# Kernel optimization log

Hardware: AMD Instinct MI355X
Metric: run time of the kernel (lower is better)

## Reference

```python
import jax, jax.numpy as jnp
import numpy as np
import math

D_MODEL = 1024
N_HEADS = 16
HEAD_DIM = 64
BATCH = 2
SEQ = 2048


def setup_inputs() -> dict:
    key = jax.random.key(0)
    ks = jax.random.split(key, 5)
    x = jax.random.normal(ks[0], (BATCH, SEQ, D_MODEL), dtype=jnp.float32)
    s = 0.02
    wq = jax.random.normal(ks[1], (D_MODEL, D_MODEL), dtype=jnp.float32) * s
    wk = jax.random.normal(ks[2], (D_MODEL, D_MODEL), dtype=jnp.float32) * s
    wv = jax.random.normal(ks[3], (D_MODEL, D_MODEL), dtype=jnp.float32) * s
    wo = jax.random.normal(ks[4], (D_MODEL, D_MODEL), dtype=jnp.float32) * s
    gammas = jnp.linspace(0.9, 0.99, N_HEADS, dtype=jnp.float32)
    return {"x": x, "wq": wq, "wk": wk, "wv": wv, "wo": wo, "gammas": gammas}


def _decay_mask(length: int, gammas: jnp.ndarray, dtype) -> jnp.ndarray:
    # [H, L, L]: gamma^(t-s) for t >= s, else 0 (causal exponential decay)
    pos = jnp.arange(length)
    diff = pos[:, None] - pos[None, :]
    causal = diff >= 0
    d = jnp.maximum(diff, 0).astype(dtype)
    g = gammas.astype(dtype)[:, None, None]
    return jnp.where(causal[None], jnp.power(g, d[None]), jnp.zeros((), dtype))


def reference(x, wq, wk, wv, wo, gammas):
    B, L, D = x.shape
    H, hd = N_HEADS, HEAD_DIM
    # torch nn.Linear: y = x @ W.T
    q = (x @ wq.T).reshape(B, L, H, hd)
    k = (x @ wk.T).reshape(B, L, H, hd)
    v = (x @ wv.T).reshape(B, L, H, hd)
    scale = 1.0 / math.sqrt(hd)
    scores = jnp.einsum('bthd,bshd->bhts', q * scale, k)  # [B,H,L,L]
    decay = _decay_mask(L, gammas, x.dtype)               # [H,L,L]
    weights = scores * decay[None]
    retained = jnp.einsum('bhts,bshd->bthd', weights, v)  # [B,L,H,hd]
    return retained.reshape(B, L, H * hd) @ wo.T
```

## Files before the change

kernel.cpp:

```cpp
#include <hip/hip_runtime.h>


typedef __attribute__((ext_vector_type(8))) short bf16x8;
typedef __attribute__((ext_vector_type(4))) float f32x4;
typedef __attribute__((ext_vector_type(16))) float f32x16;
typedef __attribute__((ext_vector_type(4))) unsigned short u16x4;
typedef __attribute__((ext_vector_type(8))) unsigned short u16x8;
typedef __attribute__((ext_vector_type(4))) unsigned int u32x4;

__device__ inline unsigned short f2bf(float f) {
    unsigned int u;
    __builtin_memcpy(&u, &f, 4);
    u += 0x7fffu + ((u >> 16) & 1u);
    return (unsigned short)(u >> 16);
}

__device__ inline f32x4 mfma16(bf16x8 a, bf16x8 b, f32x4 c) {
    return __builtin_amdgcn_mfma_f32_16x16x32_bf16(a, b, c, 0, 0, 0);
}
__device__ inline f32x16 mfma32(bf16x8 a, bf16x8 b, f32x16 c) {
    return __builtin_amdgcn_mfma_f32_32x32x16_bf16(a, b, c, 0, 0, 0);
}

__device__ inline void gl16(const unsigned short* g, unsigned short* l) {
    __builtin_amdgcn_global_load_lds(
        (const __attribute__((address_space(1))) unsigned int*)g,
        (__attribute__((address_space(3))) unsigned int*)l,
        16, 0, 0);
}

__device__ inline unsigned cvtpk(float lo, float hi) {
    unsigned r;
    asm("v_cvt_pk_bf16_f32 %0, %1, %2" : "=v"(r) : "v"(lo), "v"(hi));
    return r;
}

__global__ __launch_bounds__(256) void convert_bf16(
    const float* __restrict__ x,
    const float* __restrict__ wq, const float* __restrict__ wk,
    const float* __restrict__ wv, const float* __restrict__ wo,
    unsigned short* __restrict__ xb,
    unsigned short* __restrict__ wqb, unsigned short* __restrict__ wkb,
    unsigned short* __restrict__ wvb, unsigned short* __restrict__ wob)
{
    int cid = blockIdx.x * 256 + threadIdx.x;
    #pragma unroll
    for (int it = 0; it < 4; ++it, cid += 262144) {
        const float* src;
        unsigned short* dst;
        size_t off;
        if (cid < 524288) {
            src = x; dst = xb; off = (size_t)cid * 8;
        } else {
            const int t = cid - 524288;
            const int seg = t >> 17;
            off = (size_t)(t & 131071) * 8;
            src = seg == 0 ? wq : seg == 1 ? wk : seg == 2 ? wv : wo;
            dst = seg == 0 ? wqb : seg == 1 ? wkb : seg == 2 ? wvb : wob;
        }
        f32x4 a = *(const f32x4*)(src + off);
        f32x4 b = *(const f32x4*)(src + off + 4);
        u32x4 v = { cvtpk(a[0], a[1]), cvtpk(a[2], a[3]),
                    cvtpk(b[0], b[1]), cvtpk(b[2], b[3]) };
        *(u32x4*)(dst + off) = v;
    }
}

__global__ __launch_bounds__(256) void qkv_bf16(
    const unsigned short* __restrict__ xb,
    const unsigned short* __restrict__ wqb, const unsigned short* __restrict__ wkb,
    const unsigned short* __restrict__ wvb,
    unsigned short* __restrict__ qfr, unsigned short* __restrict__ kfr,
    unsigned short* __restrict__ vfr)
{
    __shared__ unsigned short sR[128 * 64];
    __shared__ unsigned short sL[128 * 64];

    const int z = blockIdx.z;
    const unsigned short* W = (z == 0) ? wqb : (z == 1) ? wkb : wvb;
    const unsigned short* Rs = (z < 2) ? xb : W;
    const unsigned short* Ls = (z < 2) ? W : xb;
    const int rblk = (z < 2) ? blockIdx.x : blockIdx.y;
    const int lblk = (z < 2) ? blockIdx.y : blockIdx.x;

    const int tid = threadIdx.x;
    const int l = tid & 63, w = tid >> 6;
    const int lrow = l & 15, koff4 = (l >> 4) * 4;
    const int swz = lrow & 7;
    const int wrow = (w >> 1) * 64, wcol = (w & 1) * 64;

    f32x4 acc[4][4] = {};

    const int srow = w * 32 + (l >> 3);
    const int scol = ((l & 7) ^ ((l >> 3) & 7)) * 8;
    const unsigned short* gR = Rs + (size_t)(rblk * 128 + srow) * 1024 + scol;
    const unsigned short* gL = Ls + (size_t)(lblk * 128 + srow) * 1024 + scol;
    unsigned short* lRb = sR + (w * 32) * 64;
    unsigned short* lLb = sL + (w * 32) * 64;

    for (int kk = 0; kk < 1024; kk += 64) {
        #pragma unroll
        for (int p = 0; p < 4; ++p) {
            gl16(gR + (size_t)p * 8 * 1024 + kk, lRb + p * 512);
            gl16(gL + (size_t)p * 8 * 1024 + kk, lLb + p * 512);
        }
        __syncthreads();
        #pragma unroll
        for (int kt = 0; kt < 2; ++kt) {
            bf16x8 aL[4], bR[4];
            #pragma unroll
            for (int f = 0; f < 4; ++f) {
                const int co = ((kt * 4 + (l >> 4)) ^ swz) * 8;
                aL[f] = *(const bf16x8*)&sL[(wcol + f * 16 + lrow) * 64 + co];
                bR[f] = *(const bf16x8*)&sR[(wrow + f * 16 + lrow) * 64 + co];
            }
            #pragma unroll
            for (int af = 0; af < 4; ++af)
                #pragma unroll
                for (int bf = 0; bf < 4; ++bf)
                    acc[af][bf] = mfma16(aL[af], bR[bf], acc[af][bf]);
        }
        __syncthreads();
    }

    #pragma unroll
    for (int af = 0; af < 4; ++af) {
        #pragma unroll
        for (int bf = 0; bf < 4; ++bf) {
            const int m = rblk * 128 + wrow + bf * 16 + lrow;
            const int n0 = lblk * 128 + wcol + af * 16 + koff4;
            f32x4 v = acc[af][bf];
            unsigned p0 = cvtpk(v[0], v[1]), p1 = cvtpk(v[2], v[3]);
            u16x4 val = { (unsigned short)(p0 & 0xffff), (unsigned short)(p0 >> 16),
                          (unsigned short)(p1 & 0xffff), (unsigned short)(p1 >> 16) };
            if (z < 2) {
                const int bq = m >> 11, s = m & 2047;
                const int h2 = n0 >> 6, dd = n0 & 63;
                const size_t addr = (size_t)((bq * 16 + h2) * 64 + (s >> 5)) * 2048
                                  + (size_t)(dd >> 4) * 512 + (size_t)((dd >> 3) & 1) * 256
                                  + (size_t)(s & 31) * 8 + (dd & 7);
                unsigned short* dst = z ? kfr : qfr;
                *(u16x4*)(dst + addr) = val;
            } else {
                const int h2 = m >> 6, dd = m & 63;
                const int bq = n0 >> 11, t = n0 & 2047;
                const size_t addr = (size_t)((bq * 16 + h2) * 64 + (t >> 5)) * 2048
                                  + (size_t)((dd >> 5) * 2 + ((t >> 4) & 1)) * 512
                                  + (size_t)((t >> 3) & 1) * 256
                                  + (size_t)(dd & 31) * 8 + (t & 7);
                *(u16x4*)(vfr + addr) = val;
            }
        }
    }
}

__global__ __launch_bounds__(256) void retention_paired(
    const unsigned short* __restrict__ qfr, const unsigned short* __restrict__ kfr,
    const unsigned short* __restrict__ vfr, const float* __restrict__ gammas,
    unsigned short* __restrict__ ret)
{
    __shared__ float red[3][32][64];

    const int bid = blockIdx.x;
    const int xcd = bid & 7;
    const int j = bid >> 3;
    const int m = j >> 5;
    const int p = j & 31;
    const int b = m >> 1;
    const int pi = b ? (7 - xcd) : xcd;
    const int h = (m & 1) ? (15 - pi) : pi;
    const float lg = log2f(gammas[h]);
    const int cut_i = (int)(45.0f / (-lg));
    const float gi32 = exp2f(-32.0f * lg);

    const int tid = threadIdx.x;
    const int l = tid & 63, w = tid >> 6;
    const int l31 = l & 31, hi = l >> 5;

    const size_t hbase = (size_t)((b * 16 + h) * 64) * 2048;
    const unsigned short* qfb = qfr + hbase + l * 8;
    const unsigned short* kfb = kfr + hbase + l * 8;
    const unsigned short* vfb = vfr + hbase + l * 8;

    float cf[16];
    #pragma unroll
    for (int r = 0; r < 16; ++r) {
        const int crow = (r & 3) + (hi << 2) + ((r >> 2) << 3);
        cf[r] = exp2f((float)(31 - crow) * lg);
    }

    auto ldk = [&](int sb, bf16x8* kf) {
        const unsigned short* ptr = kfb + (size_t)sb * 2048;
        #pragma unroll
        for (int kt = 0; kt < 4; ++kt) kf[kt] = *(const bf16x8*)(ptr + kt * 512);
    };
    auto ldv = [&](int sb, bf16x8* vf) {
        const unsigned short* ptr = vfb + (size_t)sb * 2048;
        #pragma unroll
        for (int i = 0; i < 4; ++i) vf[i] = *(const bf16x8*)(ptr + i * 512);
    };

    auto do_tile = [&](int tw) {
        const int tw0 = tw << 5;
        const int tq = tw0 + l31;

        bf16x8 qf[4];
        #pragma unroll
        for (int kt = 0; kt < 4; ++kt)
            qf[kt] = *(const bf16x8*)(qfb + (size_t)tw * 2048 + kt * 512);

        int sb_lo = tw0 - 31 - cut_i;
        sb_lo = (sb_lo <= 0) ? 0 : (sb_lo >> 5);

        const int n = tw - sb_lo + 1;
        const int chunk = (n + 3) >> 2;
        const int my_lo = sb_lo + w * chunk;
        int my_hi = my_lo + chunk;
        if (my_hi > tw + 1) my_hi = tw + 1;

        f32x16 acc0 = {}, acc1 = {};

        if (my_lo < my_hi) {
            float rowf = 0.125f * exp2f((float)(tq - (my_lo << 5) - 31) * lg);
            bf16x8 kc[4], vc[4], kn[4], vn[4];
            ldk(my_lo, kc);
            ldv(my_lo, vc);

            for (int sb = my_lo; sb < my_hi; ++sb) {
                if (sb + 1 < my_hi) { ldk(sb + 1, kn); ldv(sb + 1, vn); }
                f32x16 sc = {};
                __builtin_amdgcn_s_setprio(1);
                #pragma unroll
                for (int kt = 0; kt < 4; ++kt) sc = mfma32(kc[kt], qf[kt], sc);
                __builtin_amdgcn_s_setprio(0);

                float wv_[16];
                if (sb == tw) {
                    const int dtq = tq - (sb << 5);
                    #pragma unroll
                    for (int r = 0; r < 16; ++r) {
                        const int crow = (r & 3) + (hi << 2) + ((r >> 2) << 3);
                        float t_ = sc[r] * rowf * cf[r];
                        wv_[r] = (dtq >= crow) ? t_ : 0.0f;
                    }
                } else {
                    #pragma unroll
                    for (int r = 0; r < 16; ++r)
                        wv_[r] = sc[r] * rowf * cf[r];
                }
                unsigned pk_[8];
                #pragma unroll
                for (int i = 0; i < 8; ++i) pk_[i] = cvtpk(wv_[2 * i], wv_[2 * i + 1]);
                asm("v_permlane32_swap_b32 %0, %1" : "+v"(pk_[0]), "+v"(pk_[2]));
                asm("v_permlane32_swap_b32 %0, %1" : "+v"(pk_[1]), "+v"(pk_[3]));
                asm("v_permlane32_swap_b32 %0, %1" : "+v"(pk_[4]), "+v"(pk_[6]));
                asm("v_permlane32_swap_b32 %0, %1" : "+v"(pk_[5]), "+v"(pk_[7]));
                u32x4 f0v = { pk_[0], pk_[1], pk_[2], pk_[3] };
                u32x4 f1v = { pk_[4], pk_[5], pk_[6], pk_[7] };
                const bf16x8 pa0 = __builtin_bit_cast(bf16x8, f0v);
                const bf16x8 pa1 = __builtin_bit_cast(bf16x8, f1v);
                __builtin_amdgcn_s_setprio(1);
                acc0 = mfma32(pa0, vc[0], acc0);
                acc0 = mfma32(pa1, vc[1], acc0);
                acc1 = mfma32(pa0, vc[2], acc1);
                acc1 = mfma32(pa1, vc[3], acc1);
                __builtin_amdgcn_s_setprio(0);

                rowf *= gi32;
                if (sb + 1 < my_hi) {
                    #pragma unroll
                    for (int i = 0; i < 4; ++i) { kc[i] = kn[i]; vc[i] = vn[i]; }
                }
            }
        }

        if (w > 0) {
            #pragma unroll
            for (int r = 0; r < 16; ++r) {
                red[w - 1][r][l]      = acc0[r];
                red[w - 1][r + 16][l] = acc1[r];
            }
        }
        __syncthreads();
        if (w == 0) {
            #pragma unroll
            for (int jj = 0; jj < 3; ++jj)
                #pragma unroll
                for (int r = 0; r < 16; ++r) {
                    acc0[r] += red[jj][r][l];
                    acc1[r] += red[jj][r + 16][l];
                }
            #pragma unroll
            for (int r = 0; r < 16; ++r) {
                const int tl = (r & 3) + (hi << 2) + ((r >> 2) << 3);
                unsigned short* dst = ret + (size_t)(b * 2048 + tw0 + tl) * 1024 + h * 64 + l31;
                dst[0]  = f2bf(acc0[r]);
                dst[32] = f2bf(acc1[r]);
            }
        }
        __syncthreads();
    };

    do_tile(63 - p);
    do_tile(p);
}

__global__ __launch_bounds__(256) void out_bf16(
    const unsigned short* __restrict__ ret, const unsigned short* __restrict__ wob,
    float* __restrict__ out)
{
    __shared__ unsigned short sR[128 * 64];
    __shared__ unsigned short sL[128 * 64];

    const int rblk = blockIdx.x;
    const int lblk = blockIdx.y;

    const int tid = threadIdx.x;
    const int l = tid & 63, w = tid >> 6;
    const int lrow = l & 15, koff4 = (l >> 4) * 4;
    const int swz = lrow & 7;
    const int wrow = (w >> 1) * 64, wcol = (w & 1) * 64;

    f32x4 acc[4][4] = {};

    const int srow = w * 32 + (l >> 3);
    const int scol = ((l & 7) ^ ((l >> 3) & 7)) * 8;
    const unsigned short* gR = ret + (size_t)(rblk * 128 + srow) * 1024 + scol;
    const unsigned short* gL = wob + (size_t)(lblk * 128 + srow) * 1024 + scol;
    unsigned short* lRb = sR + (w * 32) * 64;
    unsigned short* lLb = sL + (w * 32) * 64;

    for (int kk = 0; kk < 1024; kk += 64) {
        #pragma unroll
        for (int p = 0; p < 4; ++p) {
            gl16(gR + (size_t)p * 8 * 1024 + kk, lRb + p * 512);
            gl16(gL + (size_t)p * 8 * 1024 + kk, lLb + p * 512);
        }
        __syncthreads();
        #pragma unroll
        for (int kt = 0; kt < 2; ++kt) {
            bf16x8 aL[4], bR[4];
            #pragma unroll
            for (int f = 0; f < 4; ++f) {
                const int co = ((kt * 4 + (l >> 4)) ^ swz) * 8;
                aL[f] = *(const bf16x8*)&sL[(wcol + f * 16 + lrow) * 64 + co];
                bR[f] = *(const bf16x8*)&sR[(wrow + f * 16 + lrow) * 64 + co];
            }
            #pragma unroll
            for (int af = 0; af < 4; ++af)
                #pragma unroll
                for (int bf = 0; bf < 4; ++bf)
                    acc[af][bf] = mfma16(aL[af], bR[bf], acc[af][bf]);
        }
        __syncthreads();
    }

    #pragma unroll
    for (int af = 0; af < 4; ++af)
        #pragma unroll
        for (int bf = 0; bf < 4; ++bf) {
            const int m = rblk * 128 + wrow + bf * 16 + lrow;
            const int n0 = lblk * 128 + wcol + af * 16 + koff4;
            *(f32x4*)(out + (size_t)m * 1024 + n0) = acc[af][bf];
        }
}

extern "C" void kernel_launch(void* const* d_in, const int* in_sizes, int n_in,
                              void* d_out, int out_size, void* d_ws, size_t ws_size,
                              hipStream_t stream) {
    const float* x      = (const float*)d_in[0];
    const float* wq     = (const float*)d_in[1];
    const float* wk     = (const float*)d_in[2];
    const float* wv     = (const float*)d_in[3];
    const float* wo     = (const float*)d_in[4];
    const float* gammas = (const float*)d_in[5];
    float* out = (float*)d_out;

    unsigned short* ws = (unsigned short*)d_ws;
    unsigned short* qf  = ws;
    unsigned short* kf  = ws + (size_t)4 * 1024 * 1024;
    unsigned short* vf  = ws + (size_t)8 * 1024 * 1024;
    unsigned short* ret = ws + (size_t)12 * 1024 * 1024;
    unsigned short* xb  = ret;
    unsigned short* wqb = ws + (size_t)16 * 1024 * 1024;
    unsigned short* wkb = ws + (size_t)17 * 1024 * 1024;
    unsigned short* wvb = ws + (size_t)18 * 1024 * 1024;
    unsigned short* wob = ws + (size_t)19 * 1024 * 1024;

    convert_bf16<<<1024, 256, 0, stream>>>(x, wq, wk, wv, wo, xb, wqb, wkb, wvb, wob);
    qkv_bf16<<<dim3(32, 8, 3), 256, 0, stream>>>(xb, wqb, wkb, wvb, qf, kf, vf);
    retention_paired<<<1024, 256, 0, stream>>>(qf, kf, vf, gammas, ret);
    out_bf16<<<dim3(32, 8), 256, 0, stream>>>(ret, wob, out);
}
```

Before: 91.11 us.

## Split paired retention tiles into one block per tile with ping-pong K/V buffers

New measurement: 93.28 us. +2.4%, slower.

```diff
diff --git a/kernel.cpp b/kernel.cpp
--- a/kernel.cpp
+++ b/kernel.cpp
@@ -154,7 +154,7 @@
     }
 }
 
-__global__ __launch_bounds__(256) void retention_paired(
+__global__ __launch_bounds__(256) void retention_single(
     const unsigned short* __restrict__ qfr, const unsigned short* __restrict__ kfr,
     const unsigned short* __restrict__ vfr, const float* __restrict__ gammas,
     unsigned short* __restrict__ ret)
@@ -163,9 +163,10 @@
 
     const int bid = blockIdx.x;
     const int xcd = bid & 7;
-    const int j = bid >> 3;
-    const int m = j >> 5;
-    const int p = j & 31;
+    const int r_ = bid >> 3;
+    const int p = r_ >> 2;
+    const int m = r_ & 3;
+    const int tw = 63 - p;
     const int b = m >> 1;
     const int pi = b ? (7 - xcd) : xcd;
     const int h = (m & 1) ? (15 - pi) : pi;
@@ -176,12 +177,19 @@
     const int tid = threadIdx.x;
     const int l = tid & 63, w = tid >> 6;
     const int l31 = l & 31, hi = l >> 5;
+    const int tw0 = tw << 5;
+    const int tq = tw0 + l31;
 
     const size_t hbase = (size_t)((b * 16 + h) * 64) * 2048;
     const unsigned short* qfb = qfr + hbase + l * 8;
     const unsigned short* kfb = kfr + hbase + l * 8;
     const unsigned short* vfb = vfr + hbase + l * 8;
 
+    bf16x8 qf[4];
+    #pragma unroll
+    for (int kt = 0; kt < 4; ++kt)
+        qf[kt] = *(const bf16x8*)(qfb + (size_t)tw * 2048 + kt * 512);
+
     float cf[16];
     #pragma unroll
     for (int r = 0; r < 16; ++r) {
@@ -189,120 +197,112 @@
         cf[r] = exp2f((float)(31 - crow) * lg);
     }
 
-    auto ldk = [&](int sb, bf16x8* kf) {
-        const unsigned short* ptr = kfb + (size_t)sb * 2048;
-        #pragma unroll
-        for (int kt = 0; kt < 4; ++kt) kf[kt] = *(const bf16x8*)(ptr + kt * 512);
-    };
-    auto ldv = [&](int sb, bf16x8* vf) {
-        const unsigned short* ptr = vfb + (size_t)sb * 2048;
-        #pragma unroll
-        for (int i = 0; i < 4; ++i) vf[i] = *(const bf16x8*)(ptr + i * 512);
-    };
-
-    auto do_tile = [&](int tw) {
-        const int tw0 = tw << 5;
-        const int tq = tw0 + l31;
-
-        bf16x8 qf[4];
-        #pragma unroll
-        for (int kt = 0; kt < 4; ++kt)
-            qf[kt] = *(const bf16x8*)(qfb + (size_t)tw * 2048 + kt * 512);
-
-        int sb_lo = tw0 - 31 - cut_i;
-        sb_lo = (sb_lo <= 0) ? 0 : (sb_lo >> 5);
-
-        const int n = tw - sb_lo + 1;
-        const int chunk = (n + 3) >> 2;
-        const int my_lo = sb_lo + w * chunk;
-        int my_hi = my_lo + chunk;
-        if (my_hi > tw + 1) my_hi = tw + 1;
-
-        f32x16 acc0 = {}, acc1 = {};
-
-        if (my_lo < my_hi) {
-            float rowf = 0.125f * exp2f((float)(tq - (my_lo << 5) - 31) * lg);
-            bf16x8 kc[4], vc[4], kn[4], vn[4];
-            ldk(my_lo, kc);
-            ldv(my_lo, vc);
-
-            for (int sb = my_lo; sb < my_hi; ++sb) {
-                if (sb + 1 < my_hi) { ldk(sb + 1, kn); ldv(sb + 1, vn); }
-                f32x16 sc = {};
-                __builtin_amdgcn_s_setprio(1);
-                #pragma unroll
-                for (int kt = 0; kt < 4; ++kt) sc = mfma32(kc[kt], qf[kt], sc);
-                __builtin_amdgcn_s_setprio(0);
-
-                float wv_[16];
-                if (sb == tw) {
-                    const int dtq = tq - (sb << 5);
-                    #pragma unroll
-                    for (int r = 0; r < 16; ++r) {
-                        const int crow = (r & 3) + (hi << 2) + ((r >> 2) << 3);
-                        float t_ = sc[r] * rowf * cf[r];
-                        wv_[r] = (dtq >= crow) ? t_ : 0.0f;
-                    }
-                } else {
-                    #pragma unroll
-                    for (int r = 0; r < 16; ++r)
-                        wv_[r] = sc[r] * rowf * cf[r];
-                }
-                unsigned pk_[8];
-                #pragma unroll
-                for (int i = 0; i < 8; ++i) pk_[i] = cvtpk(wv_[2 * i], wv_[2 * i + 1]);
-                asm("v_permlane32_swap_b32 %0, %1" : "+v"(pk_[0]), "+v"(pk_[2]));
-                asm("v_permlane32_swap_b32 %0, %1" : "+v"(pk_[1]), "+v"(pk_[3]));
-                asm("v_permlane32_swap_b32 %0, %1" : "+v"(pk_[4]), "+v"(pk_[6]));
-                asm("v_permlane32_swap_b32 %0, %1" : "+v"(pk_[5]), "+v"(pk_[7]));
-                u32x4 f0v = { pk_[0], pk_[1], pk_[2], pk_[3] };
-                u32x4 f1v = { pk_[4], pk_[5], pk_[6], pk_[7] };
-                const bf16x8 pa0 = __builtin_bit_cast(bf16x8, f0v);
-                const bf16x8 pa1 = __builtin_bit_cast(bf16x8, f1v);
-                __builtin_amdgcn_s_setprio(1);
-                acc0 = mfma32(pa0, vc[0], acc0);
-                acc0 = mfma32(pa1, vc[1], acc0);
-                acc1 = mfma32(pa0, vc[2], acc1);
-                acc1 = mfma32(pa1, vc[3], acc1);
-                __builtin_amdgcn_s_setprio(0);
-
-                rowf *= gi32;
-                if (sb + 1 < my_hi) {
-                    #pragma unroll
-                    for (int i = 0; i < 4; ++i) { kc[i] = kn[i]; vc[i] = vn[i]; }
-                }
-            }
-        }
-
-        if (w > 0) {
-            #pragma unroll
-            for (int r = 0; r < 16; ++r) {
-                red[w - 1][r][l]      = acc0[r];
-                red[w - 1][r + 16][l] = acc1[r];
-            }
-        }
-        __syncthreads();
-        if (w == 0) {
-            #pragma unroll
-            for (int jj = 0; jj < 3; ++jj)
+    int sb_lo = tw0 - 31 - cut_i;
+    sb_lo = (sb_lo <= 0) ? 0 : (sb_lo >> 5);
+
+    const int n = tw - sb_lo + 1;
+    const int chunk = (n + 3) >> 2;
+    const int my_lo = sb_lo + w * chunk;
+    int my_hi = my_lo + chunk;
+    if (my_hi > tw + 1) my_hi = tw + 1;
+
+    f32x16 acc0 = {}, acc1 = {};
+
+    if (my_lo < my_hi) {
+        float rowf = 0.125f * exp2f((float)(tq - (my_lo << 5) - 31) * lg);
+
+        bf16x8 kA[4], vA[4], kB[4], vB[4];
+
+        auto load = [&](int sb, bf16x8* kf, bf16x8* vf) {
+            const unsigned short* kp = kfb + (size_t)sb * 2048;
+            const unsigned short* vp = vfb + (size_t)sb * 2048;
+            #pragma unroll
+            for (int kt = 0; kt < 4; ++kt) kf[kt] = *(const bf16x8*)(kp + kt * 512);
+            #pragma unroll
+            for (int i = 0; i < 4; ++i) vf[i] = *(const bf16x8*)(vp + i * 512);
+        };
+
+        auto compute = [&](const bf16x8* kc, const bf16x8* vc, int sb) {
+            f32x16 sc = {};
+            __builtin_amdgcn_s_setprio(1);
+            #pragma unroll
+            for (int kt = 0; kt < 4; ++kt) sc = mfma32(kc[kt], qf[kt], sc);
+            __builtin_amdgcn_s_setprio(0);
+
+            float wv_[16];
+            if (sb == tw) {
+                const int dtq = tq - (sb << 5);
                 #pragma unroll
                 for (int r = 0; r < 16; ++r) {
-                    acc0[r] += red[jj][r][l];
-                    acc1[r] += red[jj][r + 16][l];
+                    const int crow = (r & 3) + (hi << 2) + ((r >> 2) << 3);
+                    float t_ = sc[r] * rowf * cf[r];
+                    wv_[r] = (dtq >= crow) ? t_ : 0.0f;
                 }
+            } else {
+                #pragma unroll
+                for (int r = 0; r < 16; ++r)
+                    wv_[r] = sc[r] * rowf * cf[r];
+            }
+            unsigned pk_[8];
+            #pragma unroll
+            for (int i = 0; i < 8; ++i) pk_[i] = cvtpk(wv_[2 * i], wv_[2 * i + 1]);
+            asm("v_permlane32_swap_b32 %0, %1" : "+v"(pk_[0]), "+v"(pk_[2]));
+            asm("v_permlane32_swap_b32 %0, %1" : "+v"(pk_[1]), "+v"(pk_[3]));
+            asm("v_permlane32_swap_b32 %0, %1" : "+v"(pk_[4]), "+v"(pk_[6]));
+            asm("v_permlane32_swap_b32 %0, %1" : "+v"(pk_[5]), "+v"(pk_[7]));
+            u32x4 f0v = { pk_[0], pk_[1], pk_[2], pk_[3] };
+            u32x4 f1v = { pk_[4], pk_[5], pk_[6], pk_[7] };
+            const bf16x8 pa0 = __builtin_bit_cast(bf16x8, f0v);
+            const bf16x8 pa1 = __builtin_bit_cast(bf16x8, f1v);
+            __builtin_amdgcn_s_setprio(1);
+            acc0 = mfma32(pa0, vc[0], acc0);
+            acc0 = mfma32(pa1, vc[1], acc0);
+            acc1 = mfma32(pa0, vc[2], acc1);
+            acc1 = mfma32(pa1, vc[3], acc1);
+            __builtin_amdgcn_s_setprio(0);
+            rowf *= gi32;
+        };
+
+        int sb = my_lo;
+        load(sb, kA, vA);
+        while (true) {
+            const bool moreB = (sb + 1 < my_hi);
+            if (moreB) load(sb + 1, kB, vB);
+            compute(kA, vA, sb);
+            ++sb;
+            if (!moreB) break;
+            const bool moreA = (sb + 1 < my_hi);
+            if (moreA) load(sb + 1, kA, vA);
+            compute(kB, vB, sb);
+            ++sb;
+            if (!moreA) break;
+        }
+    }
+
+    if (w > 0) {
+        #pragma unroll
+        for (int r = 0; r < 16; ++r) {
+            red[w - 1][r][l]      = acc0[r];
+            red[w - 1][r + 16][l] = acc1[r];
+        }
+    }
+    __syncthreads();
+    if (w == 0) {
+        #pragma unroll
+        for (int jj = 0; jj < 3; ++jj)
             #pragma unroll
             for (int r = 0; r < 16; ++r) {
-                const int tl = (r & 3) + (hi << 2) + ((r >> 2) << 3);
-                unsigned short* dst = ret + (size_t)(b * 2048 + tw0 + tl) * 1024 + h * 64 + l31;
-                dst[0]  = f2bf(acc0[r]);
-                dst[32] = f2bf(acc1[r]);
-            }
-        }
-        __syncthreads();
-    };
-
-    do_tile(63 - p);
-    do_tile(p);
+                acc0[r] += red[jj][r][l];
+                acc1[r] += red[jj][r + 16][l];
+            }
+        #pragma unroll
+        for (int r = 0; r < 16; ++r) {
+            const int tl = (r & 3) + (hi << 2) + ((r >> 2) << 3);
+            unsigned short* dst = ret + (size_t)(b * 2048 + tw0 + tl) * 1024 + h * 64 + l31;
+            dst[0]  = f2bf(acc0[r]);
+            dst[32] = f2bf(acc1[r]);
+        }
+    }
 }
 
 __global__ __launch_bounds__(256) void out_bf16(
@@ -389,6 +389,6 @@
 
     convert_bf16<<<1024, 256, 0, stream>>>(x, wq, wk, wv, wo, xb, wqb, wkb, wvb, wob);
     qkv_bf16<<<dim3(32, 8, 3), 256, 0, stream>>>(xb, wqb, wkb, wvb, qf, kf, vf);
-    retention_paired<<<1024, 256, 0, stream>>>(qf, kf, vf, gammas, ret);
+    retention_single<<<2048, 256, 0, stream>>>(qf, kf, vf, gammas, ret);
     out_bf16<<<dim3(32, 8), 256, 0, stream>>>(ret, wob, out);
 }
```
